# Kernel tuning notes

Measured on AMD Instinct MI355X. Metric: run time of the kernel, lower is better.

## Reference

```python
import jax, jax.numpy as jnp
import numpy as np

N_NODES = 100000
N_EDGES = 1600000
IN_DIM = 128
HID = 96
N_CLASSES = 16
BN_EPS = 1e-5
GIN_EPS = 0.0  # DGL GINConv default init_eps=0, learn_eps=False


def setup_inputs() -> dict:
    key = jax.random.key(0)
    ks = jax.random.split(key, 16)
    d = {}
    d["h"] = jax.random.normal(ks[0], (N_NODES, IN_DIM), dtype=jnp.float32)
    d["src"] = jax.random.randint(ks[1], (N_EDGES,), 0, N_NODES, dtype=jnp.int32)
    d["dst"] = jax.random.randint(ks[2], (N_EDGES,), 0, N_NODES, dtype=jnp.int32)
    # embedding_h: Linear(input_dim, hidden)
    d["W_emb"] = jax.random.normal(ks[3], (IN_DIM, HID), dtype=jnp.float32) / np.sqrt(IN_DIM)
    d["b_emb"] = jnp.zeros((HID,), dtype=jnp.float32)
    # GIN layer 1: MLP(1 layer) Linear(hid,hid) + BN(hid)
    d["W1"] = jax.random.normal(ks[4], (HID, HID), dtype=jnp.float32) / np.sqrt(HID)
    d["b1"] = jnp.zeros((HID,), dtype=jnp.float32)
    d["g1"] = jnp.ones((HID,), dtype=jnp.float32)
    d["be1"] = jnp.zeros((HID,), dtype=jnp.float32)
    # GIN layer 2
    d["W2"] = jax.random.normal(ks[5], (HID, HID), dtype=jnp.float32) / np.sqrt(HID)
    d["b2"] = jnp.zeros((HID,), dtype=jnp.float32)
    d["g2"] = jnp.ones((HID,), dtype=jnp.float32)
    d["be2"] = jnp.zeros((HID,), dtype=jnp.float32)
    # readout: Linear(hid, n_classes)
    d["Wr"] = jax.random.normal(ks[6], (HID, N_CLASSES), dtype=jnp.float32) / np.sqrt(HID)
    d["br"] = jnp.zeros((N_CLASSES,), dtype=jnp.float32)
    return d


def _gin_layer(h, src, dst, W, b, gamma, beta):
    # sum aggregation over incoming edges: agg[v] = sum_{(u,v) in E} h[u]
    agg = jax.ops.segment_sum(h[src], dst, num_segments=N_NODES)
    z = ((1.0 + GIN_EPS) * h + agg) @ W + b           # MLP (single linear)
    mu = jnp.mean(z, axis=0)                            # BatchNorm1d (batch stats)
    var = jnp.var(z, axis=0)
    z = (z - mu) * jax.lax.rsqrt(var + BN_EPS) * gamma + beta
    return jax.nn.relu(z)


def reference(h, src, dst, W_emb, b_emb, W1, b1, g1, be1, W2, b2, g2, be2, Wr, br):
    h = h @ W_emb + b_emb                               # embedding_h
    h = _gin_layer(h, src, dst, W1, b1, g1, be1)        # dropout treated as identity (eval)
    h = _gin_layer(h, src, dst, W2, b2, g2, be2)
    logits = h @ Wr + br                                # readout
    return jax.nn.log_softmax(logits, axis=1)
```

## Files before the change

### kernel.cpp

```cpp
#include <hip/hip_runtime.h>
#include <cmath>

#define N_NODES 100000
#define N_EDGES 1600000
#define IN_DIM 128
#define HID 96
#define NCLS 16
#define NB_GATH 2048

#define BSHIFT 7
#define BNODES 128
#define NBUK 782
#define TILE_E 8192
#define NBLK_E 196
#define NBLK_Q 24
#define NBLK_R 4

typedef unsigned int uint;
typedef unsigned short ushort;
typedef __attribute__((ext_vector_type(8))) short short8v;
typedef __attribute__((ext_vector_type(4))) float float4v;

__device__ __forceinline__ ushort f2bf(float x) {
    uint b = __float_as_uint(x);
    uint r = (b + 0x7FFFu + ((b >> 16) & 1u)) >> 16;
    return (ushort)r;
}
__device__ __forceinline__ float bf2f(ushort u) {
    return __uint_as_float(((uint)u) << 16);
}
__device__ __forceinline__ float bf_lo(uint w) { return __uint_as_float(w << 16); }
__device__ __forceinline__ float bf_hi(uint w) { return __uint_as_float(w & 0xFFFF0000u); }
__device__ __forceinline__ uint pack2bf(float a, float b) {
    return (uint)f2bf(a) | ((uint)f2bf(b) << 16);
}

__device__ __forceinline__ int tile_of(int blk) {
    int xcd = blk & 7, slot = blk >> 3;
    return (xcd < NBLK_R) ? xcd * (NBLK_Q + 1) + slot
                          : NBLK_R * (NBLK_Q + 1) + (xcd - NBLK_R) * NBLK_Q + slot;
}

__global__ __launch_bounds__(256) void wfuse(const float* __restrict__ W_emb,
                                             const float* __restrict__ W1,
                                             const float* __restrict__ b_emb,
                                             float* __restrict__ Wf,
                                             float* __restrict__ bf) {
    __shared__ float W1s[HID * HID];
    for (int i = threadIdx.x; i < HID * HID / 4; i += 256)
        ((float4*)W1s)[i] = ((const float4*)W1)[i];
    __syncthreads();
    int idx = blockIdx.x * 256 + threadIdx.x;
    if (idx < IN_DIM * HID) {
        int i = idx / HID, j = idx - (idx / HID) * HID;
        float acc = 0.f;
        for (int k = 0; k < HID; ++k)
            acc = fmaf(W_emb[(size_t)i * HID + k], W1s[k * HID + j], acc);
        Wf[idx] = acc;
    }
    if (idx < HID) {
        float acc = 0.f;
        for (int k = 0; k < HID; ++k)
            acc = fmaf(b_emb[k], W1s[k * HID + idx], acc);
        bf[idx] = acc;
    }
}

__global__ __launch_bounds__(384) void gemm_l1(const float* __restrict__ X,
                                               const float* __restrict__ W,
                                               const float* __restrict__ bias,
                                               ushort* __restrict__ outB) {
    constexpr int K = IN_DIM, KPAD = K + 8;
    __shared__ ushort A_s[96 * KPAD];
    __shared__ ushort W_t[96 * KPAD];
    __shared__ float bs[HID];
    if (threadIdx.x < HID) bs[threadIdx.x] = bias[threadIdx.x];

    const int rbase = blockIdx.x * 96;
    for (int c = threadIdx.x; c < 96 * (K / 8); c += 384) {
        int row = c / (K / 8), ko = (c - row * (K / 8)) * 8;
        int gr = min(rbase + row, N_NODES - 1);
        const float* xp = X + (size_t)gr * K + ko;
        float4 v0 = *(const float4*)xp;
        float4 v1 = *(const float4*)(xp + 4);
        uint4 p;
        p.x = pack2bf(v0.x, v0.y);
        p.y = pack2bf(v0.z, v0.w);
        p.z = pack2bf(v1.x, v1.y);
        p.w = pack2bf(v1.z, v1.w);
        *(uint4*)&A_s[row * KPAD + ko] = p;
    }
    for (int j = threadIdx.x; j < K * HID; j += 384) {
        int k = j / HID, n = j - k * HID;
        W_t[n * KPAD + k] = f2bf(W[j]);
    }
    __syncthreads();

    const int lane = threadIdx.x & 63, w = threadIdx.x >> 6;
    const int ar = lane & 15, kg = lane >> 4;
    float4v acc[6] = {};
    const ushort* ap = &A_s[(w * 16 + ar) * KPAD + kg * 8];
    const ushort* bp = &W_t[ar * KPAD + kg * 8];
#pragma unroll
    for (int kc = 0; kc < K / 32; ++kc) {
        short8v af = *(const short8v*)(ap + kc * 32);
#pragma unroll
        for (int ct = 0; ct < 6; ++ct) {
            short8v bfv = *(const short8v*)(bp + ct * 16 * KPAD + kc * 32);
            acc[ct] = __builtin_amdgcn_mfma_f32_16x16x32_bf16(af, bfv, acc[ct], 0, 0, 0);
        }
    }
#pragma unroll
    for (int ct = 0; ct < 6; ++ct) {
        int col = ct * 16 + ar;
        float bb = bs[col];
#pragma unroll
        for (int i = 0; i < 4; ++i) {
            int grow = rbase + w * 16 + kg * 4 + i;
            if (grow < N_NODES)
                outB[(size_t)grow * HID + col] = f2bf(acc[ct][i] + bb);
        }
    }
}

__global__ __launch_bounds__(384) void gemm_l2(const ushort* __restrict__ X,
                                               const float* __restrict__ W,
                                               const float* __restrict__ scale,
                                               const float* __restrict__ shift,
                                               ushort* __restrict__ outB) {
    constexpr int K = HID, KPAD = K + 8;
    __shared__ ushort A_s[96 * KPAD];
    __shared__ ushort W_t[96 * KPAD];
    __shared__ float scs[HID], shs[HID];
    if (threadIdx.x < HID) {
        scs[threadIdx.x] = scale[threadIdx.x];
        shs[threadIdx.x] = shift[threadIdx.x];
    }
    __syncthreads();

    const int rbase = blockIdx.x * 96;
    for (int c = threadIdx.x; c < 96 * (K / 8); c += 384) {
        int row = c / (K / 8), ko = (c - row * (K / 8)) * 8;
        int gr = min(rbase + row, N_NODES - 1);
        uint4 u = *(const uint4*)(X + (size_t)gr * K + ko);
        float4 sA = *(const float4*)&scs[ko], sB = *(const float4*)&scs[ko + 4];
        float4 hA = *(const float4*)&shs[ko], hB = *(const float4*)&shs[ko + 4];
        float v0 = fmaxf(fmaf(bf_lo(u.x), sA.x, hA.x), 0.f);
        float v1 = fmaxf(fmaf(bf_hi(u.x), sA.y, hA.y), 0.f);
        float v2 = fmaxf(fmaf(bf_lo(u.y), sA.z, hA.z), 0.f);
        float v3 = fmaxf(fmaf(bf_hi(u.y), sA.w, hA.w), 0.f);
        float v4 = fmaxf(fmaf(bf_lo(u.z), sB.x, hB.x), 0.f);
        float v5 = fmaxf(fmaf(bf_hi(u.z), sB.y, hB.y), 0.f);
        float v6 = fmaxf(fmaf(bf_lo(u.w), sB.z, hB.z), 0.f);
        float v7 = fmaxf(fmaf(bf_hi(u.w), sB.w, hB.w), 0.f);
        uint4 p;
        p.x = pack2bf(v0, v1);
        p.y = pack2bf(v2, v3);
        p.z = pack2bf(v4, v5);
        p.w = pack2bf(v6, v7);
        *(uint4*)&A_s[row * KPAD + ko] = p;
    }
    for (int j = threadIdx.x; j < K * HID; j += 384) {
        int k = j / HID, n = j - k * HID;
        W_t[n * KPAD + k] = f2bf(W[j]);
    }
    __syncthreads();

    const int lane = threadIdx.x & 63, w = threadIdx.x >> 6;
    const int ar = lane & 15, kg = lane >> 4;
    float4v acc[6] = {};
    const ushort* ap = &A_s[(w * 16 + ar) * KPAD + kg * 8];
    const ushort* bp = &W_t[ar * KPAD + kg * 8];
#pragma unroll
    for (int kc = 0; kc < K / 32; ++kc) {
        short8v af = *(const short8v*)(ap + kc * 32);
#pragma unroll
        for (int ct = 0; ct < 6; ++ct) {
            short8v bfv = *(const short8v*)(bp + ct * 16 * KPAD + kc * 32);
            acc[ct] = __builtin_amdgcn_mfma_f32_16x16x32_bf16(af, bfv, acc[ct], 0, 0, 0);
        }
    }
#pragma unroll
    for (int ct = 0; ct < 6; ++ct) {
        int col = ct * 16 + ar;
#pragma unroll
        for (int i = 0; i < 4; ++i) {
            int grow = rbase + w * 16 + kg * 4 + i;
            if (grow < N_NODES)
                outB[(size_t)grow * HID + col] = f2bf(acc[ct][i]);
        }
    }
}

__global__ __launch_bounds__(256) void bin_hist(const int* __restrict__ dst,
                                                int* __restrict__ bcnt) {
    int tile = tile_of(blockIdx.x);
    int beg = tile * TILE_E, end = min(beg + TILE_E, N_EDGES);
    __shared__ int cnt[NBUK];
    for (int b = threadIdx.x; b < NBUK; b += 256) cnt[b] = 0;
    __syncthreads();
    for (int i = beg + threadIdx.x * 4; i < end; i += 256 * 4) {
        int4 d = *(const int4*)(dst + i);
        atomicAdd(&cnt[d.x >> BSHIFT], 1);
        atomicAdd(&cnt[d.y >> BSHIFT], 1);
        atomicAdd(&cnt[d.z >> BSHIFT], 1);
        atomicAdd(&cnt[d.w >> BSHIFT], 1);
    }
    __syncthreads();
    for (int b = threadIdx.x; b < NBUK; b += 256) bcnt[(size_t)b * NBLK_E + tile] = cnt[b];
}

__global__ __launch_bounds__(256) void bin_scanA(const int* __restrict__ bcnt,
                                                 int* __restrict__ boff,
                                                 int* __restrict__ btot) {
    int bin = blockIdx.x, t = threadIdx.x;
    __shared__ int tmp[256];
    int v = (t < NBLK_E) ? bcnt[(size_t)bin * NBLK_E + t] : 0;
    tmp[t] = v;
    __syncthreads();
    for (int off = 1; off < 256; off <<= 1) {
        int a = (t >= off) ? tmp[t - off] : 0;
        __syncthreads();
        tmp[t] += a;
        __syncthreads();
    }
    if (t < NBLK_E) boff[(size_t)bin * NBLK_E + t] = tmp[t] - v;
    if (t == NBLK_E - 1) btot[bin] = tmp[t];
}

__global__ __launch_bounds__(1024) void exscan782(const int* __restrict__ in,
                                                  int* __restrict__ out,
                                                  int sentinel) {
    int t = threadIdx.x;
    __shared__ int tmp[1024];
    int v = (t < NBUK) ? in[t] : 0;
    tmp[t] = v;
    __syncthreads();
    for (int off = 1; off < 1024; off <<= 1) {
        int a = (t >= off) ? tmp[t - off] : 0;
        __syncthreads();
        tmp[t] += a;
        __syncthreads();
    }
    if (t < NBUK) out[t] = tmp[t] - v;
    if (t == 0 && sentinel >= 0) out[NBUK] = sentinel;
}

__global__ __launch_bounds__(256) void bin_scatter(const int* __restrict__ src,
                                                   const int* __restrict__ dst,
                                                   const int* __restrict__ bbase,
                                                   const int* __restrict__ boff,
                                                   int* __restrict__ ebuf) {
    int tile = tile_of(blockIdx.x);
    int beg = tile * TILE_E, end = min(beg + TILE_E, N_EDGES);
    __shared__ int curs[NBUK];
    for (int b = threadIdx.x; b < NBUK; b += 256)
        curs[b] = bbase[b] + boff[(size_t)b * NBLK_E + tile];
    __syncthreads();
    for (int i = beg + threadIdx.x * 4; i < end; i += 256 * 4) {
        int4 d = *(const int4*)(dst + i);
        int4 s = *(const int4*)(src + i);
#pragma unroll
        for (int e = 0; e < 4; ++e) {
            int dv = e == 0 ? d.x : e == 1 ? d.y : e == 2 ? d.z : d.w;
            int sv = e == 0 ? s.x : e == 1 ? s.y : e == 2 ? s.z : s.w;
            int p = atomicAdd(&curs[dv >> BSHIFT], 1);
            ebuf[p] = (sv << BSHIFT) | (dv & (BNODES - 1));
        }
    }
}

__global__ __launch_bounds__(256) void bucket_hist(const int* __restrict__ ebuf,
                                                   const int* __restrict__ bbase,
                                                   int* __restrict__ deg,
                                                   int* __restrict__ bsumsB) {
    int b = blockIdx.x;
    int lo = b << BSHIFT;
    __shared__ int cnt[BNODES];
    if (threadIdx.x < BNODES) cnt[threadIdx.x] = 0;
    __syncthreads();
    int beg = bbase[b], end = bbase[b + 1];
    for (int i = beg + threadIdx.x; i < end; i += 256)
        atomicAdd(&cnt[ebuf[i] & (BNODES - 1)], 1);
    __syncthreads();
    if (threadIdx.x < BNODES && lo + threadIdx.x < N_NODES)
        deg[lo + threadIdx.x] = cnt[threadIdx.x];
    if (threadIdx.x < 64) cnt[threadIdx.x] += cnt[threadIdx.x + 64];
    __syncthreads();
    if (threadIdx.x < 32) cnt[threadIdx.x] += cnt[threadIdx.x + 32];
    __syncthreads();
    if (threadIdx.x < 16) cnt[threadIdx.x] += cnt[threadIdx.x + 16];
    __syncthreads();
    if (threadIdx.x == 0) {
        int s = 0;
        for (int i = 0; i < 16; ++i) s += cnt[i];
        bsumsB[b] = s;
    }
}

__global__ __launch_bounds__(128) void scan_final(const int* __restrict__ deg,
                                                  const int* __restrict__ boffs,
                                                  int* __restrict__ rp) {
    int b = blockIdx.x, t = threadIdx.x;
    int i = b * BNODES + t;
    int val = (i < N_NODES) ? deg[i] : 0;
    __shared__ int tmp[BNODES];
    tmp[t] = val;
    __syncthreads();
    for (int off = 1; off < BNODES; off <<= 1) {
        int a = (t >= off) ? tmp[t - off] : 0;
        __syncthreads();
        tmp[t] += a;
        __syncthreads();
    }
    int excl = tmp[t] - val + boffs[b];
    if (i < N_NODES) {
        rp[i] = excl;
        if (i == N_NODES - 1) rp[N_NODES] = excl + val;
    }
}

__global__ __launch_bounds__(256) void bucket_place(const int* __restrict__ ebuf,
                                                    const int* __restrict__ bbase,
                                                    const int* __restrict__ rp,
                                                    int* __restrict__ cols) {
    int b = blockIdx.x;
    int lo = b << BSHIFT;
    __shared__ int cur[BNODES];
    if (threadIdx.x < BNODES)
        cur[threadIdx.x] = (lo + threadIdx.x < N_NODES) ? rp[lo + threadIdx.x] : 0;
    __syncthreads();
    int beg = bbase[b], end = bbase[b + 1];
    for (int i = beg + threadIdx.x; i < end; i += 256) {
        int v = ebuf[i];
        int p = atomicAdd(&cur[v & (BNODES - 1)], 1);
        cols[p] = v >> BSHIFT;
    }
}

#define GLANES 24
#define GNODES 8

__global__ __launch_bounds__(192) void gather_stats(const ushort* __restrict__ T,
                                                    const int* __restrict__ rp,
                                                    const int* __restrict__ cols,
                                                    const float* __restrict__ bias,
                                                    ushort* __restrict__ z,
                                                    float* __restrict__ psums,
                                                    float* __restrict__ psq) {
    const int q = threadIdx.x % GLANES;
    const int rs = threadIdx.x / GLANES;
    const float4 bias4 = ((const float4*)bias)[q];
    float4 s = make_float4(0.f, 0.f, 0.f, 0.f);
    float4 sq = make_float4(0.f, 0.f, 0.f, 0.f);

#define ADDROW(u)                                                              \
    {                                                                          \
        ushort4 w = *(const ushort4*)(T + (size_t)(u) * HID + q * 4);          \
        a.x += bf2f(w.x); a.y += bf2f(w.y);                                    \
        a.z += bf2f(w.z); a.w += bf2f(w.w);                                    \
    }

    for (int v = blockIdx.x * GNODES + rs; v < N_NODES; v += NB_GATH * GNODES) {
        float4 a = bias4;
        ADDROW(v);
        int beg = rp[v], end = rp[v + 1];
        int j = beg;
        for (; j + 3 < end; j += 4) {
            int u0 = cols[j], u1 = cols[j + 1], u2 = cols[j + 2], u3 = cols[j + 3];
            ADDROW(u0); ADDROW(u1); ADDROW(u2); ADDROW(u3);
        }
        for (; j < end; ++j) ADDROW(cols[j]);

        uint2 o;
        o.x = pack2bf(a.x, a.y);
        o.y = pack2bf(a.z, a.w);
        *(uint2*)(z + (size_t)v * HID + q * 4) = o;
        s.x += a.x; s.y += a.y; s.z += a.z; s.w += a.w;
        sq.x = fmaf(a.x, a.x, sq.x);
        sq.y = fmaf(a.y, a.y, sq.y);
        sq.z = fmaf(a.z, a.z, sq.z);
        sq.w = fmaf(a.w, a.w, sq.w);
    }
#undef ADDROW

    __shared__ float4 ls[GNODES][GLANES], lq[GNODES][GLANES];
    ls[rs][q] = s;
    lq[rs][q] = sq;
    __syncthreads();
    if (threadIdx.x < GLANES) {
        float4 S = ls[0][threadIdx.x], Q = lq[0][threadIdx.x];
#pragma unroll
        for (int i = 1; i < GNODES; ++i) {
            S.x += ls[i][threadIdx.x].x; S.y += ls[i][threadIdx.x].y;
            S.z += ls[i][threadIdx.x].z; S.w += ls[i][threadIdx.x].w;
            Q.x += lq[i][threadIdx.x].x; Q.y += lq[i][threadIdx.x].y;
            Q.z += lq[i][threadIdx.x].z; Q.w += lq[i][threadIdx.x].w;
        }
        ((float4*)(psums + (size_t)blockIdx.x * HID))[threadIdx.x] = S;
        ((float4*)(psq + (size_t)blockIdx.x * HID))[threadIdx.x] = Q;
    }
}

__global__ __launch_bounds__(384) void bn_finalize(const float* __restrict__ psums,
                                                   const float* __restrict__ psq,
                                                   const float* __restrict__ g,
                                                   const float* __restrict__ be,
                                                   float* __restrict__ scale,
                                                   float* __restrict__ shift) {
    int c = threadIdx.x % 96, h = threadIdx.x / 96;
    float S = 0.f, Q = 0.f;
    for (int b = h * (NB_GATH / 4); b < (h + 1) * (NB_GATH / 4); ++b) {
        S += psums[(size_t)b * HID + c];
        Q += psq[(size_t)b * HID + c];
    }
    __shared__ float lS[4][96], lQ[4][96];
    lS[h][c] = S;
    lQ[h][c] = Q;
    __syncthreads();
    if (threadIdx.x < 96) {
        S = lS[0][c] + lS[1][c] + lS[2][c] + lS[3][c];
        Q = lQ[0][c] + lQ[1][c] + lQ[2][c] + lQ[3][c];
        float mu = S * (1.0f / N_NODES);
        float var = Q * (1.0f / N_NODES) - mu * mu;
        float rstd = rsqrtf(var + 1e-5f);
        float sc = g[c] * rstd;
        scale[c] = sc;
        shift[c] = be[c] - mu * sc;
    }
}

__global__ __launch_bounds__(256) void readout_kernel(const ushort* __restrict__ X,
                                                      const float* __restrict__ scale,
                                                      const float* __restrict__ shift,
                                                      const float* __restrict__ Wr,
                                                      const float* __restrict__ br,
                                                      float* __restrict__ out) {
    __shared__ float Ws[HID * NCLS];
    __shared__ float XL[16 * 97];
    __shared__ float scs[HID], shs[HID], bs[NCLS];
    for (int i = threadIdx.x; i < HID * NCLS / 4; i += 256)
        ((float4*)Ws)[i] = ((const float4*)Wr)[i];
    if (threadIdx.x < HID) {
        scs[threadIdx.x] = scale[threadIdx.x];
        shs[threadIdx.x] = shift[threadIdx.x];
    }
    if (threadIdx.x < NCLS) bs[threadIdx.x] = br[threadIdx.x];

    int rr = threadIdx.x >> 4, t = threadIdx.x & 15;
    for (int tile = blockIdx.x; tile < N_NODES / 16; tile += gridDim.x) {
        int rbase = tile * 16;
        __syncthreads();
        if (threadIdx.x < 192) {
            int base = threadIdx.x * 8;
            int row = base / HID, col = base - (base / HID) * HID;
            uint4 w = *(const uint4*)(X + (size_t)rbase * HID + base);
            float v[8] = {bf_lo(w.x), bf_hi(w.x), bf_lo(w.y), bf_hi(w.y),
                          bf_lo(w.z), bf_hi(w.z), bf_lo(w.w), bf_hi(w.w)};
#pragma unroll
            for (int e = 0; e < 8; ++e)
                XL[row * 97 + col + e] = fmaxf(fmaf(v[e], scs[col + e], shs[col + e]), 0.f);
        }
        __syncthreads();
        float acc = bs[t];
        const float* xrow = &XL[rr * 97];
#pragma unroll 4
        for (int k = 0; k < HID; ++k) acc = fmaf(xrow[k], Ws[k * NCLS + t], acc);
        float m = acc;
#pragma unroll
        for (int off = 8; off; off >>= 1) m = fmaxf(m, __shfl_xor(m, off, 16));
        float e = expf(acc - m);
        float sum = e;
#pragma unroll
        for (int off = 8; off; off >>= 1) sum += __shfl_xor(sum, off, 16);
        float lse = m + logf(sum);
        out[(size_t)rbase * NCLS + threadIdx.x] = acc - lse;
    }
}

extern "C" void kernel_launch(void* const* d_in, const int* in_sizes, int n_in,
                              void* d_out, int out_size, void* d_ws, size_t ws_size,
                              hipStream_t stream) {
    const float* h     = (const float*)d_in[0];
    const int*   src   = (const int*)d_in[1];
    const int*   dst   = (const int*)d_in[2];
    const float* W_emb = (const float*)d_in[3];
    const float* b_emb = (const float*)d_in[4];
    const float* W1    = (const float*)d_in[5];
    const float* b1    = (const float*)d_in[6];
    const float* g1    = (const float*)d_in[7];
    const float* be1   = (const float*)d_in[8];
    const float* W2    = (const float*)d_in[9];
    const float* b2    = (const float*)d_in[10];
    const float* g2    = (const float*)d_in[11];
    const float* be2   = (const float*)d_in[12];
    const float* Wr    = (const float*)d_in[13];
    const float* br    = (const float*)d_in[14];

    const size_t nh = (size_t)N_NODES * HID;
    ushort* z    = (ushort*)d_ws;
    ushort* T    = z + nh;
    int* deg     = (int*)(T + nh);
    int* rp      = deg + N_NODES;
    int* cols    = rp + N_NODES + 1;
    int* ebuf    = cols + N_EDGES;
    int* bcnt    = ebuf + N_EDGES;
    int* boff    = bcnt + NBUK * NBLK_E;
    int* btot    = boff + NBUK * NBLK_E;
    int* bbase   = btot + NBUK;
    int* bsumsB  = bbase + NBUK + 1;
    int* boffs   = bsumsB + NBUK;
    float* psums = (float*)(boffs + NBUK);
    float* psq   = psums + (size_t)NB_GATH * HID;
    float* scale = psq + (size_t)NB_GATH * HID;
    float* shift = scale + HID;
    float* Wf    = shift + HID;
    float* bf    = Wf + IN_DIM * HID;

    const int blkT = (N_NODES + 95) / 96;

    bin_hist<<<NBLK_E, 256, 0, stream>>>(dst, bcnt);
    bin_scanA<<<NBUK, 256, 0, stream>>>(bcnt, boff, btot);
    exscan782<<<1, 1024, 0, stream>>>(btot, bbase, N_EDGES);
    bin_scatter<<<NBLK_E, 256, 0, stream>>>(src, dst, bbase, boff, ebuf);
    bucket_hist<<<NBUK, 256, 0, stream>>>(ebuf, bbase, deg, bsumsB);
    exscan782<<<1, 1024, 0, stream>>>(bsumsB, boffs, -1);
    scan_final<<<NBUK, 128, 0, stream>>>(deg, boffs, rp);
    bucket_place<<<NBUK, 256, 0, stream>>>(ebuf, bbase, rp, cols);
    wfuse<<<(IN_DIM * HID + 255) / 256, 256, 0, stream>>>(W_emb, W1, b_emb, Wf, bf);

    gemm_l1<<<blkT, 384, 0, stream>>>(h, Wf, bf, T);
    gather_stats<<<NB_GATH, 192, 0, stream>>>(T, rp, cols, b1, z, psums, psq);
    bn_finalize<<<1, 384, 0, stream>>>(psums, psq, g1, be1, scale, shift);

    gemm_l2<<<blkT, 384, 0, stream>>>(z, W2, scale, shift, T);
    gather_stats<<<NB_GATH, 192, 0, stream>>>(T, rp, cols, b2, z, psums, psq);
    bn_finalize<<<1, 384, 0, stream>>>(psums, psq, g2, be2, scale, shift);

    readout_kernel<<<2048, 256, 0, stream>>>(z, scale, shift, Wr, br, (float*)d_out);
}
```

Before: 323.4 us.

## Fuse bucket histogram, scan and placement into one CSR-build kernel

Merges bucket_hist, the second exscan, scan_final and bucket_place into a single bucket_finalize kernel. Since bucket bases already equal the prefix of edge counts, each block computes its local node offsets from bbase plus an in-block scan. This removes three launches and the deg/boffs round trips through global memory. It also raises the gather grid from 2048 to 2560 blocks and adds an 8-way unrolled neighbor loop, at the cost of more registers.

```diff
diff --git a/kernel.cpp b/kernel.cpp
--- a/kernel.cpp
+++ b/kernel.cpp
@@ -6,7 +6,7 @@
 #define IN_DIM 128
 #define HID 96
 #define NCLS 16
-#define NB_GATH 2048
+#define NB_GATH 2560
 
 #define BSHIFT 7
 #define BNODES 128
@@ -229,8 +229,7 @@
 }
 
 __global__ __launch_bounds__(1024) void exscan782(const int* __restrict__ in,
-                                                  int* __restrict__ out,
-                                                  int sentinel) {
+                                                  int* __restrict__ out) {
     int t = threadIdx.x;
     __shared__ int tmp[1024];
     int v = (t < NBUK) ? in[t] : 0;
@@ -243,7 +242,7 @@
         __syncthreads();
     }
     if (t < NBUK) out[t] = tmp[t] - v;
-    if (t == 0 && sentinel >= 0) out[NBUK] = sentinel;
+    if (t == 0) out[NBUK] = N_EDGES;
 }
 
 __global__ __launch_bounds__(256) void bin_scatter(const int* __restrict__ src,
@@ -270,67 +269,39 @@
     }
 }
 
-__global__ __launch_bounds__(256) void bucket_hist(const int* __restrict__ ebuf,
-                                                   const int* __restrict__ bbase,
-                                                   int* __restrict__ deg,
-                                                   int* __restrict__ bsumsB) {
+__global__ __launch_bounds__(256) void bucket_finalize(const int* __restrict__ ebuf,
+                                                       const int* __restrict__ bbase,
+                                                       int* __restrict__ rp,
+                                                       int* __restrict__ cols) {
     int b = blockIdx.x;
     int lo = b << BSHIFT;
     __shared__ int cnt[BNODES];
+    __shared__ int cur[BNODES];
     if (threadIdx.x < BNODES) cnt[threadIdx.x] = 0;
     __syncthreads();
     int beg = bbase[b], end = bbase[b + 1];
     for (int i = beg + threadIdx.x; i < end; i += 256)
         atomicAdd(&cnt[ebuf[i] & (BNODES - 1)], 1);
     __syncthreads();
-    if (threadIdx.x < BNODES && lo + threadIdx.x < N_NODES)
-        deg[lo + threadIdx.x] = cnt[threadIdx.x];
-    if (threadIdx.x < 64) cnt[threadIdx.x] += cnt[threadIdx.x + 64];
-    __syncthreads();
-    if (threadIdx.x < 32) cnt[threadIdx.x] += cnt[threadIdx.x + 32];
-    __syncthreads();
-    if (threadIdx.x < 16) cnt[threadIdx.x] += cnt[threadIdx.x + 16];
-    __syncthreads();
-    if (threadIdx.x == 0) {
-        int s = 0;
-        for (int i = 0; i < 16; ++i) s += cnt[i];
-        bsumsB[b] = s;
-    }
-}
-
-__global__ __launch_bounds__(128) void scan_final(const int* __restrict__ deg,
-                                                  const int* __restrict__ boffs,
-                                                  int* __restrict__ rp) {
-    int b = blockIdx.x, t = threadIdx.x;
-    int i = b * BNODES + t;
-    int val = (i < N_NODES) ? deg[i] : 0;
-    __shared__ int tmp[BNODES];
-    tmp[t] = val;
+    int t = threadIdx.x;
+    int val = (t < BNODES) ? cnt[t] : 0;
+    if (t < BNODES) cur[t] = val;
     __syncthreads();
     for (int off = 1; off < BNODES; off <<= 1) {
-        int a = (t >= off) ? tmp[t - off] : 0;
-        __syncthreads();
-        tmp[t] += a;
-        __syncthreads();
-    }
-    int excl = tmp[t] - val + boffs[b];
-    if (i < N_NODES) {
-        rp[i] = excl;
-        if (i == N_NODES - 1) rp[N_NODES] = excl + val;
-    }
-}
-
-__global__ __launch_bounds__(256) void bucket_place(const int* __restrict__ ebuf,
-                                                    const int* __restrict__ bbase,
-                                                    const int* __restrict__ rp,
-                                                    int* __restrict__ cols) {
-    int b = blockIdx.x;
-    int lo = b << BSHIFT;
-    __shared__ int cur[BNODES];
-    if (threadIdx.x < BNODES)
-        cur[threadIdx.x] = (lo + threadIdx.x < N_NODES) ? rp[lo + threadIdx.x] : 0;
-    __syncthreads();
-    int beg = bbase[b], end = bbase[b + 1];
+        int a = (t < BNODES && t >= off) ? cur[t - off] : 0;
+        __syncthreads();
+        if (t < BNODES) cur[t] += a;
+        __syncthreads();
+    }
+    if (t < BNODES) {
+        int excl = beg + cur[t] - val;
+        if (lo + t < N_NODES) {
+            rp[lo + t] = excl;
+            if (lo + t == N_NODES - 1) rp[N_NODES] = N_EDGES;
+        }
+        cur[t] = excl;
+    }
+    __syncthreads();
     for (int i = beg + threadIdx.x; i < end; i += 256) {
         int v = ebuf[i];
         int p = atomicAdd(&cur[v & (BNODES - 1)], 1);
@@ -366,6 +337,12 @@
         ADDROW(v);
         int beg = rp[v], end = rp[v + 1];
         int j = beg;
+        for (; j + 7 < end; j += 8) {
+            int u0 = cols[j], u1 = cols[j + 1], u2 = cols[j + 2], u3 = cols[j + 3];
+            int u4 = cols[j + 4], u5 = cols[j + 5], u6 = cols[j + 6], u7 = cols[j + 7];
+            ADDROW(u0); ADDROW(u1); ADDROW(u2); ADDROW(u3);
+            ADDROW(u4); ADDROW(u5); ADDROW(u6); ADDROW(u7);
+        }
         for (; j + 3 < end; j += 4) {
             int u0 = cols[j], u1 = cols[j + 1], u2 = cols[j + 2], u3 = cols[j + 3];
             ADDROW(u0); ADDROW(u1); ADDROW(u2); ADDROW(u3);
@@ -500,17 +477,14 @@
     const size_t nh = (size_t)N_NODES * HID;
     ushort* z    = (ushort*)d_ws;
     ushort* T    = z + nh;
-    int* deg     = (int*)(T + nh);
-    int* rp      = deg + N_NODES;
+    int* rp      = (int*)(T + nh);
     int* cols    = rp + N_NODES + 1;
     int* ebuf    = cols + N_EDGES;
     int* bcnt    = ebuf + N_EDGES;
     int* boff    = bcnt + NBUK * NBLK_E;
     int* btot    = boff + NBUK * NBLK_E;
     int* bbase   = btot + NBUK;
-    int* bsumsB  = bbase + NBUK + 1;
-    int* boffs   = bsumsB + NBUK;
-    float* psums = (float*)(boffs + NBUK);
+    float* psums = (float*)(bbase + NBUK + 1);
     float* psq   = psums + (size_t)NB_GATH * HID;
     float* scale = psq + (size_t)NB_GATH * HID;
     float* shift = scale + HID;
@@ -521,12 +495,9 @@
 
     bin_hist<<<NBLK_E, 256, 0, stream>>>(dst, bcnt);
     bin_scanA<<<NBUK, 256, 0, stream>>>(bcnt, boff, btot);
-    exscan782<<<1, 1024, 0, stream>>>(btot, bbase, N_EDGES);
+    exscan782<<<1, 1024, 0, stream>>>(btot, bbase);
     bin_scatter<<<NBLK_E, 256, 0, stream>>>(src, dst, bbase, boff, ebuf);
-    bucket_hist<<<NBUK, 256, 0, stream>>>(ebuf, bbase, deg, bsumsB);
-    exscan782<<<1, 1024, 0, stream>>>(bsumsB, boffs, -1);
-    scan_final<<<NBUK, 128, 0, stream>>>(deg, boffs, rp);
-    bucket_place<<<NBUK, 256, 0, stream>>>(ebuf, bbase, rp, cols);
+    bucket_finalize<<<NBUK, 256, 0, stream>>>(ebuf, bbase, rp, cols);
     wfuse<<<(IN_DIM * HID + 255) / 256, 256, 0, stream>>>(W_emb, W1, b_emb, Wf, bf);
 
     gemm_l1<<<blkT, 384, 0, stream>>>(h, Wf, bf, T);
```

Result: faster. 310.9 us (-3.8%).
